# Optimization experiments

Hardware: AMD Instinct MI355X
Metric: run time of the kernel (lower is better)

Reference implementation:

```python
import jax, jax.numpy as jnp
import numpy as np

B, C, W, H = 16, 256, 32, 32
HEAD, NREG = 4, 1
D = C // HEAD
N = W * H


def setup_inputs() -> dict:
    key = jax.random.key(0)
    ks = jax.random.split(key, 11)
    return {
        "x": jax.random.normal(ks[0], (B, C, W, H), jnp.float32),
        "Wq": jax.random.normal(ks[1], (C, C), jnp.float32) * 0.05,
        "bq": jax.random.normal(ks[2], (C,), jnp.float32) * 0.05,
        "Wk": jax.random.normal(ks[3], (C, C), jnp.float32) * 0.05,
        "bk": jax.random.normal(ks[4], (C,), jnp.float32) * 0.05,
        "Wv": jax.random.normal(ks[5], (C, C), jnp.float32) * 0.05,
        "bv": jax.random.normal(ks[6], (C,), jnp.float32) * 0.05,
        "rel_h": jax.random.normal(ks[7], (1, HEAD, D, 1, H), jnp.float32),
        "rel_w": jax.random.normal(ks[8], (1, HEAD, D, W, 1), jnp.float32),
        "reg_qk": jax.random.normal(ks[9], (NREG, N, N), jnp.float32),
        "reg_v": jax.random.normal(ks[10], (NREG, D, N), jnp.float32),
    }


def reference(x, Wq, bq, Wk, bk, Wv, bv, rel_h, rel_w, reg_qk, reg_v):
    b, c, w, h = x.shape
    head = rel_h.shape[1]
    d = c // head
    n = w * h
    xf = x.reshape(b, c, n)  # flatten spatial; 1x1 conv == channel matmul
    q = (jnp.einsum('oc,bcn->bon', Wq, xf) + bq[:, None]).reshape(b, head, d, n)
    k = (jnp.einsum('oc,bcn->bon', Wk, xf) + bk[:, None]).reshape(b, head, d, n)
    v = (jnp.einsum('oc,bcn->bon', Wv, xf) + bv[:, None]).reshape(b, head, d, n)
    # content-content: q^T k -> [b, head, n, n]
    cc = jnp.einsum('bhdn,bhdm->bhnm', q, k)
    # relative position: (rel_h + rel_w) broadcast-summed to [1,head,d,w,h] -> [head,d,n]
    pos = (rel_h + rel_w).reshape(head, d, n)
    # pos^T @ q -> [b, head, n, n]
    cp = jnp.einsum('hdn,bhdm->bhnm', pos, q)
    energy = cc + cp  # [b, head, n, n]
    # pack register tokens along the head axis
    energy = jnp.concatenate(
        [energy, jnp.broadcast_to(reg_qk[None], (b,) + reg_qk.shape)], axis=1)
    vcat = jnp.concatenate(
        [v, jnp.broadcast_to(reg_v[None], (b,) + reg_v.shape)], axis=1)
    attn = jax.nn.softmax(energy, axis=-1)  # [b, head+nreg, n, n]
    # out = v @ attn^T : [b, g, d, n]
    out = jnp.einsum('bgdn,bgmn->bgdm', vcat, attn)
    # unpack: keep only the real heads
    out = out[:, :head].reshape(b, c, w, h)
    return out
```

## Files before the change

### kernel.cpp

```cpp
#include <hip/hip_runtime.h>

#define BB 16
#define CH 256
#define NH 4
#define DH 64
#define NN 1024

typedef _Float16 f16x8 __attribute__((ext_vector_type(8)));
typedef float f32x4 __attribute__((ext_vector_type(4)));
typedef float f32x16 __attribute__((ext_vector_type(16)));
typedef unsigned int uint32x4 __attribute__((ext_vector_type(4)));

__device__ __forceinline__ unsigned short f2h(float x) {
    _Float16 h = (_Float16)x;
    return __builtin_bit_cast(unsigned short, h);
}

__device__ __forceinline__ unsigned cvtpk(float a, float b) {
    auto r = __builtin_amdgcn_cvt_pkrtz(a, b);
    return __builtin_bit_cast(unsigned, r);
}

__global__ __launch_bounds__(256) void prep_kernel(
    const float* __restrict__ Wq, const float* __restrict__ Wk, const float* __restrict__ Wv,
    unsigned short* __restrict__ Wh)
{
    int idx = blockIdx.x * 256 + threadIdx.x;
    if (idx >= 3 * CH * CH) return;
    int p = idx >> 16, oc = idx & 65535;
    const float* W = (p == 0) ? Wq : ((p == 1) ? Wk : Wv);
    Wh[idx] = f2h(W[oc]);
}

__global__ __launch_bounds__(256) void xt_kernel(
    const float* __restrict__ x, unsigned short* __restrict__ xT)
{
    const int b = blockIdx.z, c0 = blockIdx.y * 32, n0 = blockIdx.x * 32;
    __shared__ float T[32][33];
    const int t = threadIdx.x;
    {
        int c = t >> 3, n4 = (t & 7) * 4;
        float4 v4 = *(const float4*)&x[((size_t)b * CH + c0 + c) * NN + n0 + n4];
        T[c][n4 + 0] = v4.x; T[c][n4 + 1] = v4.y;
        T[c][n4 + 2] = v4.z; T[c][n4 + 3] = v4.w;
    }
    __syncthreads();
    {
        int n = t >> 3, c4 = (t & 7) * 4;
        ushort4 o;
        o.x = f2h(T[c4 + 0][n]); o.y = f2h(T[c4 + 1][n]);
        o.z = f2h(T[c4 + 2][n]); o.w = f2h(T[c4 + 3][n]);
        *(ushort4*)&xT[((size_t)b * NN + n0 + n) * CH + c0 + c4] = o;
    }
}

__global__ __launch_bounds__(256) void pos_kernel(
    const float* __restrict__ rel_h, const float* __restrict__ rel_w,
    unsigned short* __restrict__ pT)
{
    int idx = blockIdx.x * 256 + threadIdx.x;
    if (idx >= NH * NN * DH) return;
    int d = idx & 63, n = (idx >> 6) & (NN - 1), h = idx >> 16;
    float val = rel_w[(h * DH + d) * 32 + (n >> 5)] + rel_h[(h * DH + d) * 32 + (n & 31)];
    pT[idx] = f2h(val);
}

__global__ __launch_bounds__(256) void proj_kernel(
    const unsigned short* __restrict__ xT,
    const unsigned short* __restrict__ Wh,
    const float* __restrict__ bq, const float* __restrict__ bk, const float* __restrict__ bv,
    unsigned short* __restrict__ kF, unsigned short* __restrict__ vF)
{
    const int bz = blockIdx.z;
    const int b = bz / 3, p = bz % 3;
    const int jt = blockIdx.x;
    const int ot = blockIdx.y;
    const int n0 = jt * 64;
    const int o0 = ot * 64;
    const float* bias = (p == 0) ? bq : ((p == 1) ? bk : bv);

    __shared__ __align__(16) unsigned short Xs[64][72];
    __shared__ __align__(16) unsigned short Whs[64][72];
    __shared__ __align__(16) unsigned short Img[8192];

    const int tid = threadIdx.x;
    const int wid = tid >> 6, lane = tid & 63;
    const int g = lane >> 4, lr = lane & 15;
    const int l31 = lane & 31, hi = lane >> 5;

    const unsigned short* xb  = xT + (size_t)b * NN * CH;
    const unsigned short* Whp = Wh + (size_t)p * CH * CH;

    const f32x4 z4 = {0.f, 0.f, 0.f, 0.f};
    f32x4 acc[4] = {z4, z4, z4, z4};

    for (int cs = 0; cs < 4; ++cs) {
        const int c0 = cs * 64;
        __syncthreads();
        #pragma unroll
        for (int rep = 0; rep < 2; ++rep) {
            int f = rep * 256 + tid;
            int r = f >> 3, s = f & 7;
            *(uint4*)&Xs[r][s * 8]  = *(const uint4*)&xb[(size_t)(n0 + r) * CH + c0 + s * 8];
            *(uint4*)&Whs[r][s * 8] = *(const uint4*)&Whp[(size_t)(o0 + r) * CH + c0 + s * 8];
        }
        __syncthreads();
        #pragma unroll
        for (int ks = 0; ks < 2; ++ks) {
            f16x8 ah = *(const f16x8*)&Whs[wid * 16 + lr][ks * 32 + g * 8];
            #pragma unroll
            for (int fc = 0; fc < 4; ++fc) {
                f16x8 bx = *(const f16x8*)&Xs[fc * 16 + lr][ks * 32 + g * 8];
                acc[fc] = __builtin_amdgcn_mfma_f32_16x16x32_f16(ah, bx, acc[fc], 0, 0, 0);
            }
        }
    }

    float bb[4];
    #pragma unroll
    for (int rr = 0; rr < 4; ++rr) bb[rr] = bias[o0 + wid * 16 + g * 4 + rr];

    const int bh = b * NH + ot;

    if (p < 2) {
        const float scale = (p == 0) ? 1.44269504088896f : 1.0f;
        const int qoff = (p == 0) ? 8 : 0;
        #pragma unroll
        for (int fc = 0; fc < 4; ++fc)
            #pragma unroll
            for (int rr = 0; rr < 4; ++rr) {
                int jl = fc * 16 + lr;
                int dd = wid * 16 + g * 4 + rr;
                Img[jl * 128 + ((((dd >> 3) + qoff) ^ (jl & 15)) << 3) + (dd & 7)] =
                    f2h((acc[fc][rr] + bb[rr]) * scale);
            }
        __syncthreads();
        const int ks = ((p == 0) ? 4 : 0) + wid;
        #pragma unroll
        for (int grp = 0; grp < 2; ++grp) {
            int row = grp * 32 + l31;
            int slot = ks * 2 + hi;
            uint4 v = *(const uint4*)&Img[row * 128 + ((slot ^ (row & 15)) << 3)];
            size_t dst = ((((size_t)bh * 16 + jt) * 8 + ks) * 2 + grp) * 512 + (size_t)lane * 8;
            *(uint4*)&kF[dst] = v;
        }
    } else {
        #pragma unroll
        for (int fc = 0; fc < 4; ++fc)
            #pragma unroll
            for (int rr = 0; rr < 4; ++rr) {
                int d  = wid * 16 + g * 4 + rr;
                int jl = fc * 16 + lr;
                int vc = jl >> 3, c4 = (jl >> 2) & 1, c = jl & 3;
                int vM = ((vc >> 1) << 2) + (vc & 1) + ((d >> 5) << 4);
                Img[(d & 31) * 128 + ((((vM >> 1) + c4) ^ (d & 15)) << 3) + ((vM & 1) << 2) + c] =
                    f2h(acc[fc][rr] + bb[rr]);
            }
        __syncthreads();
        const int u = wid;
        #pragma unroll
        for (int which = 0; which < 2; ++which) {
            int slot = which * 8 + u * 2 + hi;
            int row = l31;
            uint4 v = *(const uint4*)&Img[row * 128 + ((slot ^ (row & 15)) << 3)];
            size_t dst = ((((size_t)bh * 16 + jt) * 4 + u) * 2 + which) * 512 + (size_t)lane * 8;
            *(uint4*)&vF[dst] = v;
        }
    }
}

__global__ __launch_bounds__(256, 2) void attn_kernel(
    const unsigned short* __restrict__ pT,
    const unsigned short* __restrict__ kF, const unsigned short* __restrict__ vF,
    float* __restrict__ out)
{
    const int wg = blockIdx.x;
    const int bh = (wg & 7) * 8 + ((wg >> 3) & 7);
    const int it = wg >> 6;
    const int b = bh >> 2, h = bh & 3;
    const int i0 = it * 128;

    __shared__ __align__(16) float Epi[64 * 132];
    __shared__ __align__(16) float Lbuf[128];
    __shared__ float ScBuf[4][32];

    const int tid = threadIdx.x;
    const int wid = tid >> 6, lane = tid & 63;
    const int l31 = lane & 31, hi = lane >> 5;

    const unsigned short* pTb = pT + (size_t)h * NN * DH;

    const unsigned short* kFb = kF + (size_t)bh * 16 * 8192 + (size_t)lane * 8;
    const unsigned short* vFb = vF + (size_t)bh * 16 * 4096 + (size_t)lane * 8;

    f16x8 bQ[8];
    {
        const int i = i0 + wid * 32 + l31;
        const unsigned short* qck = kFb + (size_t)(it * 2 + (wid >> 1)) * 8192;
        #pragma unroll
        for (int ksp = 0; ksp < 4; ++ksp) {
            bQ[ksp] = *(const f16x8*)(qck + (((4 + ksp) * 2 + (wid & 1)) * 512));
            bQ[4 + ksp] = *(const f16x8*)&pTb[(size_t)i * DH + ksp * 16 + hi * 8];
        }
    }

    f32x16 O0 = {}, O1 = {};
    float m_run = -1e30f, l_run = 0.f;

    for (int t = 0; t < 16; ++t) {
        const unsigned short* kt = kFb + (size_t)t * 8192;
        const unsigned short* vt = vFb + (size_t)t * 4096;

        f16x8 a0[8], a1[8];
        #pragma unroll
        for (int ks = 0; ks < 8; ++ks) {
            a0[ks] = *(const f16x8*)(kt + ks * 1024);
            a1[ks] = *(const f16x8*)(kt + ks * 1024 + 512);
        }
        f16x8 vf0[4], vf1[4];
        #pragma unroll
        for (int u = 0; u < 4; ++u) {
            vf0[u] = *(const f16x8*)(vt + u * 1024);
            vf1[u] = *(const f16x8*)(vt + u * 1024 + 512);
        }

        f32x16 s0 = {}, s1 = {};
        __builtin_amdgcn_s_setprio(1);
        #pragma unroll
        for (int ks = 0; ks < 8; ++ks) {
            s0 = __builtin_amdgcn_mfma_f32_32x32x16_f16(a0[ks], bQ[ks], s0, 0, 0, 0);
            s1 = __builtin_amdgcn_mfma_f32_32x32x16_f16(a1[ks], bQ[ks], s1, 0, 0, 0);
        }
        __builtin_amdgcn_s_setprio(0);

        float fm = s0[0];
        #pragma unroll
        for (int r = 1; r < 16; ++r) fm = fmaxf(fm, s0[r]);
        #pragma unroll
        for (int r = 0; r < 16; ++r) fm = fmaxf(fm, s1[r]);

        if (!__all(fm <= m_run + 8.f)) {
            float fmf = fmaxf(fm, __shfl_xor(fm, 32));
            float mn = fmaxf(m_run, fmf);
            float sc = exp2f(m_run - mn);
            m_run = mn;
            l_run *= sc;
            if (lane < 32) ScBuf[wid][lane] = sc;
            #pragma unroll
            for (int r = 0; r < 16; ++r) {
                int irow = (r & 3) + 8 * (r >> 2) + 4 * hi;
                float scv = ScBuf[wid][irow];
                O0[r] *= scv; O1[r] *= scv;
            }
        }

        unsigned c0[8], c1[8];
        float ps = 0.f;
        #pragma unroll
        for (int m = 0; m < 8; ++m) {
            float pa = exp2f(s0[2 * m]     - m_run);
            float pb = exp2f(s0[2 * m + 1] - m_run);
            float pc = exp2f(s1[2 * m]     - m_run);
            float pd = exp2f(s1[2 * m + 1] - m_run);
            ps += (pa + pb) + (pc + pd);
            c0[m] = cvtpk(pa, pb);
            c1[m] = cvtpk(pc, pd);
        }
        l_run += ps;

        f16x8 pA[2][2];
        #pragma unroll
        for (int js = 0; js < 2; ++js) {
            unsigned* c = js ? c1 : c0;
            #pragma unroll
            for (int ksi = 0; ksi < 2; ++ksi) {
                uint32x4 w = { c[ksi * 4 + 0], c[ksi * 4 + 1], c[ksi * 4 + 2], c[ksi * 4 + 3] };
                pA[js][ksi] = __builtin_bit_cast(f16x8, w);
            }
        }

        __builtin_amdgcn_s_setprio(1);
        #pragma unroll
        for (int js = 0; js < 2; ++js) {
            #pragma unroll
            for (int ksi = 0; ksi < 2; ++ksi) {
                int u = js * 2 + ksi;
                O0 = __builtin_amdgcn_mfma_f32_32x32x16_f16(pA[js][ksi], vf0[u], O0, 0, 0, 0);
                O1 = __builtin_amdgcn_mfma_f32_32x32x16_f16(pA[js][ksi], vf1[u], O1, 0, 0, 0);
            }
        }
        __builtin_amdgcn_s_setprio(0);
    }

    float l_full = l_run + __shfl_xor(l_run, 32);
    float invl = 1.0f / l_full;
    if (lane < 32) Lbuf[wid * 32 + lane] = invl;
    #pragma unroll
    for (int r = 0; r < 16; ++r) {
        int irow = (r & 3) + 8 * (r >> 2) + 4 * hi;
        int ilocal = wid * 32 + irow;
        Epi[(l31) * 132 + ilocal]      = O0[r];
        Epi[(32 + l31) * 132 + ilocal] = O1[r];
    }
    __syncthreads();
    float* ob = out + ((size_t)b * CH + h * DH) * NN + i0;
    #pragma unroll
    for (int rep = 0; rep < 8; ++rep) {
        int f = rep * 256 + tid;
        int d = f >> 5, q = f & 31;
        float4 v4 = *(const float4*)&Epi[d * 132 + q * 4];
        float4 iv = *(const float4*)&Lbuf[q * 4];
        v4.x *= iv.x; v4.y *= iv.y; v4.z *= iv.z; v4.w *= iv.w;
        *(float4*)&ob[(size_t)d * NN + q * 4] = v4;
    }
}

extern "C" void kernel_launch(void* const* d_in, const int* in_sizes, int n_in,
                              void* d_out, int out_size, void* d_ws, size_t ws_size,
                              hipStream_t stream) {
    const float* x     = (const float*)d_in[0];
    const float* Wq    = (const float*)d_in[1];
    const float* bq    = (const float*)d_in[2];
    const float* Wk    = (const float*)d_in[3];
    const float* bk    = (const float*)d_in[4];
    const float* Wv    = (const float*)d_in[5];
    const float* bv    = (const float*)d_in[6];
    const float* rel_h = (const float*)d_in[7];
    const float* rel_w = (const float*)d_in[8];
    float* out = (float*)d_out;

    unsigned short* kF = (unsigned short*)d_ws;
    unsigned short* vF = kF + (size_t)8388608;
    unsigned short* pT = vF + (size_t)4194304;
    unsigned short* xT = pT + (size_t)262144;
    unsigned short* Wh = xT + (size_t)4194304;

    prep_kernel<<<dim3((3 * CH * CH + 255) / 256), 256, 0, stream>>>(Wq, Wk, Wv, Wh);
    xt_kernel<<<dim3(NN / 32, CH / 32, BB), 256, 0, stream>>>(x, xT);
    pos_kernel<<<dim3((NH * NN * DH + 255) / 256), 256, 0, stream>>>(rel_h, rel_w, pT);
    proj_kernel<<<dim3(NN / 64, CH / 64, BB * 3), 256, 0, stream>>>(
        xT, Wh, bq, bk, bv, kF, vF);
    attn_kernel<<<dim3(512), 256, 0, stream>>>(pT, kF, vF, out);
}
```

Measured before the change: 78.85 us.

## Fuse weight conversion and position embedding into projection and attention kernels

Removes the separate weight fp16 conversion and position-table kernels. The projection kernel now converts fp32 weights on the fly and computes Q, K and V for one x tile in a single block. That block loads its x tile once into a larger shared buffer and reuses it across all three projections. The attention kernel builds the position fragment directly from rel_h/rel_w. This cuts two launches and the x reloads, but each projection block does three times the work, launches a third as many blocks, and issues scattered scalar loads for the position terms.

```diff
diff --git a/kernel.cpp b/kernel.cpp
--- a/kernel.cpp
+++ b/kernel.cpp
@@ -19,17 +19,6 @@
 __device__ __forceinline__ unsigned cvtpk(float a, float b) {
     auto r = __builtin_amdgcn_cvt_pkrtz(a, b);
     return __builtin_bit_cast(unsigned, r);
-}
-
-__global__ __launch_bounds__(256) void prep_kernel(
-    const float* __restrict__ Wq, const float* __restrict__ Wk, const float* __restrict__ Wv,
-    unsigned short* __restrict__ Wh)
-{
-    int idx = blockIdx.x * 256 + threadIdx.x;
-    if (idx >= 3 * CH * CH) return;
-    int p = idx >> 16, oc = idx & 65535;
-    const float* W = (p == 0) ? Wq : ((p == 1) ? Wk : Wv);
-    Wh[idx] = f2h(W[oc]);
 }
 
 __global__ __launch_bounds__(256) void xt_kernel(
@@ -54,124 +43,130 @@
     }
 }
 
-__global__ __launch_bounds__(256) void pos_kernel(
-    const float* __restrict__ rel_h, const float* __restrict__ rel_w,
-    unsigned short* __restrict__ pT)
-{
-    int idx = blockIdx.x * 256 + threadIdx.x;
-    if (idx >= NH * NN * DH) return;
-    int d = idx & 63, n = (idx >> 6) & (NN - 1), h = idx >> 16;
-    float val = rel_w[(h * DH + d) * 32 + (n >> 5)] + rel_h[(h * DH + d) * 32 + (n & 31)];
-    pT[idx] = f2h(val);
-}
-
 __global__ __launch_bounds__(256) void proj_kernel(
     const unsigned short* __restrict__ xT,
-    const unsigned short* __restrict__ Wh,
+    const float* __restrict__ Wq, const float* __restrict__ Wk, const float* __restrict__ Wv,
     const float* __restrict__ bq, const float* __restrict__ bk, const float* __restrict__ bv,
     unsigned short* __restrict__ kF, unsigned short* __restrict__ vF)
 {
-    const int bz = blockIdx.z;
-    const int b = bz / 3, p = bz % 3;
     const int jt = blockIdx.x;
     const int ot = blockIdx.y;
-    const int n0 = jt * 64;
-    const int o0 = ot * 64;
-    const float* bias = (p == 0) ? bq : ((p == 1) ? bk : bv);
-
-    __shared__ __align__(16) unsigned short Xs[64][72];
-    __shared__ __align__(16) unsigned short Whs[64][72];
-    __shared__ __align__(16) unsigned short Img[8192];
+    const int b  = blockIdx.z;
+    const int n0 = jt * 64, o0 = ot * 64;
+
+    __shared__ __align__(16) unsigned short Xs[64][264];
+    __shared__ __align__(16) unsigned short WhImg[8192];
+    unsigned short (*Whs)[72] = (unsigned short (*)[72])WhImg;
+    unsigned short* Img = WhImg;
 
     const int tid = threadIdx.x;
     const int wid = tid >> 6, lane = tid & 63;
     const int g = lane >> 4, lr = lane & 15;
     const int l31 = lane & 31, hi = lane >> 5;
 
-    const unsigned short* xb  = xT + (size_t)b * NN * CH;
-    const unsigned short* Whp = Wh + (size_t)p * CH * CH;
-
+    const unsigned short* xb = xT + (size_t)b * NN * CH;
+
+    #pragma unroll
+    for (int rep = 0; rep < 8; ++rep) {
+        int f = rep * 256 + tid;
+        int n = f >> 5, s = f & 31;
+        *(uint4*)&Xs[n][s * 8] = *(const uint4*)&xb[(size_t)(n0 + n) * CH + s * 8];
+    }
+
+    const int bh = b * NH + ot;
     const f32x4 z4 = {0.f, 0.f, 0.f, 0.f};
-    f32x4 acc[4] = {z4, z4, z4, z4};
-
-    for (int cs = 0; cs < 4; ++cs) {
-        const int c0 = cs * 64;
+
+    for (int p = 0; p < 3; ++p) {
+        const float* Wp   = (p == 0) ? Wq : ((p == 1) ? Wk : Wv);
+        const float* bias = (p == 0) ? bq : ((p == 1) ? bk : bv);
+
+        f32x4 acc[4] = {z4, z4, z4, z4};
+
+        for (int cs = 0; cs < 4; ++cs) {
+            const int c0 = cs * 64;
+            __syncthreads();
+            #pragma unroll
+            for (int rep = 0; rep < 2; ++rep) {
+                int f = rep * 256 + tid;
+                int r = f >> 3, s = f & 7;
+                const float* src = &Wp[(size_t)(o0 + r) * CH + c0 + s * 8];
+                float4 w0 = *(const float4*)src;
+                float4 w1 = *(const float4*)(src + 4);
+                ushort4 ha, hb;
+                ha.x = f2h(w0.x); ha.y = f2h(w0.y); ha.z = f2h(w0.z); ha.w = f2h(w0.w);
+                hb.x = f2h(w1.x); hb.y = f2h(w1.y); hb.z = f2h(w1.z); hb.w = f2h(w1.w);
+                *(ushort4*)&Whs[r][s * 8]     = ha;
+                *(ushort4*)&Whs[r][s * 8 + 4] = hb;
+            }
+            __syncthreads();
+            #pragma unroll
+            for (int ks = 0; ks < 2; ++ks) {
+                f16x8 ah = *(const f16x8*)&Whs[wid * 16 + lr][ks * 32 + g * 8];
+                #pragma unroll
+                for (int fc = 0; fc < 4; ++fc) {
+                    f16x8 bx = *(const f16x8*)&Xs[fc * 16 + lr][c0 + ks * 32 + g * 8];
+                    acc[fc] = __builtin_amdgcn_mfma_f32_16x16x32_f16(ah, bx, acc[fc], 0, 0, 0);
+                }
+            }
+        }
+
+        float bb[4];
+        #pragma unroll
+        for (int rr = 0; rr < 4; ++rr) bb[rr] = bias[o0 + wid * 16 + g * 4 + rr];
+
         __syncthreads();
-        #pragma unroll
-        for (int rep = 0; rep < 2; ++rep) {
-            int f = rep * 256 + tid;
-            int r = f >> 3, s = f & 7;
-            *(uint4*)&Xs[r][s * 8]  = *(const uint4*)&xb[(size_t)(n0 + r) * CH + c0 + s * 8];
-            *(uint4*)&Whs[r][s * 8] = *(const uint4*)&Whp[(size_t)(o0 + r) * CH + c0 + s * 8];
-        }
-        __syncthreads();
-        #pragma unroll
-        for (int ks = 0; ks < 2; ++ks) {
-            f16x8 ah = *(const f16x8*)&Whs[wid * 16 + lr][ks * 32 + g * 8];
-            #pragma unroll
-            for (int fc = 0; fc < 4; ++fc) {
-                f16x8 bx = *(const f16x8*)&Xs[fc * 16 + lr][ks * 32 + g * 8];
-                acc[fc] = __builtin_amdgcn_mfma_f32_16x16x32_f16(ah, bx, acc[fc], 0, 0, 0);
-            }
-        }
-    }
-
-    float bb[4];
-    #pragma unroll
-    for (int rr = 0; rr < 4; ++rr) bb[rr] = bias[o0 + wid * 16 + g * 4 + rr];
-
-    const int bh = b * NH + ot;
-
-    if (p < 2) {
-        const float scale = (p == 0) ? 1.44269504088896f : 1.0f;
-        const int qoff = (p == 0) ? 8 : 0;
-        #pragma unroll
-        for (int fc = 0; fc < 4; ++fc)
-            #pragma unroll
-            for (int rr = 0; rr < 4; ++rr) {
-                int jl = fc * 16 + lr;
-                int dd = wid * 16 + g * 4 + rr;
-                Img[jl * 128 + ((((dd >> 3) + qoff) ^ (jl & 15)) << 3) + (dd & 7)] =
-                    f2h((acc[fc][rr] + bb[rr]) * scale);
-            }
-        __syncthreads();
-        const int ks = ((p == 0) ? 4 : 0) + wid;
-        #pragma unroll
-        for (int grp = 0; grp < 2; ++grp) {
-            int row = grp * 32 + l31;
-            int slot = ks * 2 + hi;
-            uint4 v = *(const uint4*)&Img[row * 128 + ((slot ^ (row & 15)) << 3)];
-            size_t dst = ((((size_t)bh * 16 + jt) * 8 + ks) * 2 + grp) * 512 + (size_t)lane * 8;
-            *(uint4*)&kF[dst] = v;
-        }
-    } else {
-        #pragma unroll
-        for (int fc = 0; fc < 4; ++fc)
-            #pragma unroll
-            for (int rr = 0; rr < 4; ++rr) {
-                int d  = wid * 16 + g * 4 + rr;
-                int jl = fc * 16 + lr;
-                int vc = jl >> 3, c4 = (jl >> 2) & 1, c = jl & 3;
-                int vM = ((vc >> 1) << 2) + (vc & 1) + ((d >> 5) << 4);
-                Img[(d & 31) * 128 + ((((vM >> 1) + c4) ^ (d & 15)) << 3) + ((vM & 1) << 2) + c] =
-                    f2h(acc[fc][rr] + bb[rr]);
-            }
-        __syncthreads();
-        const int u = wid;
-        #pragma unroll
-        for (int which = 0; which < 2; ++which) {
-            int slot = which * 8 + u * 2 + hi;
-            int row = l31;
-            uint4 v = *(const uint4*)&Img[row * 128 + ((slot ^ (row & 15)) << 3)];
-            size_t dst = ((((size_t)bh * 16 + jt) * 4 + u) * 2 + which) * 512 + (size_t)lane * 8;
-            *(uint4*)&vF[dst] = v;
+
+        if (p < 2) {
+            const float scale = (p == 0) ? 1.44269504088896f : 1.0f;
+            const int qoff = (p == 0) ? 8 : 0;
+            #pragma unroll
+            for (int fc = 0; fc < 4; ++fc)
+                #pragma unroll
+                for (int rr = 0; rr < 4; ++rr) {
+                    int jl = fc * 16 + lr;
+                    int dd = wid * 16 + g * 4 + rr;
+                    Img[jl * 128 + ((((dd >> 3) + qoff) ^ (jl & 15)) << 3) + (dd & 7)] =
+                        f2h((acc[fc][rr] + bb[rr]) * scale);
+                }
+            __syncthreads();
+            const int ks = ((p == 0) ? 4 : 0) + wid;
+            #pragma unroll
+            for (int grp = 0; grp < 2; ++grp) {
+                int row = grp * 32 + l31;
+                int slot = ks * 2 + hi;
+                uint4 v = *(const uint4*)&Img[row * 128 + ((slot ^ (row & 15)) << 3)];
+                size_t dst = ((((size_t)bh * 16 + jt) * 8 + ks) * 2 + grp) * 512 + (size_t)lane * 8;
+                *(uint4*)&kF[dst] = v;
+            }
+        } else {
+            #pragma unroll
+            for (int fc = 0; fc < 4; ++fc)
+                #pragma unroll
+                for (int rr = 0; rr < 4; ++rr) {
+                    int d  = wid * 16 + g * 4 + rr;
+                    int jl = fc * 16 + lr;
+                    int vc = jl >> 3, c4 = (jl >> 2) & 1, c = jl & 3;
+                    int vM = ((vc >> 1) << 2) + (vc & 1) + ((d >> 5) << 4);
+                    Img[(d & 31) * 128 + ((((vM >> 1) + c4) ^ (d & 15)) << 3) + ((vM & 1) << 2) + c] =
+                        f2h(acc[fc][rr] + bb[rr]);
+                }
+            __syncthreads();
+            const int u = wid;
+            #pragma unroll
+            for (int which = 0; which < 2; ++which) {
+                int slot = which * 8 + u * 2 + hi;
+                int row = l31;
+                uint4 v = *(const uint4*)&Img[row * 128 + ((slot ^ (row & 15)) << 3)];
+                size_t dst = ((((size_t)bh * 16 + jt) * 4 + u) * 2 + which) * 512 + (size_t)lane * 8;
+                *(uint4*)&vF[dst] = v;
+            }
         }
     }
 }
 
 __global__ __launch_bounds__(256, 2) void attn_kernel(
-    const unsigned short* __restrict__ pT,
     const unsigned short* __restrict__ kF, const unsigned short* __restrict__ vF,
+    const float* __restrict__ rel_h, const float* __restrict__ rel_w,
     float* __restrict__ out)
 {
     const int wg = blockIdx.x;
@@ -188,19 +183,25 @@
     const int wid = tid >> 6, lane = tid & 63;
     const int l31 = lane & 31, hi = lane >> 5;
 
-    const unsigned short* pTb = pT + (size_t)h * NN * DH;
-
     const unsigned short* kFb = kF + (size_t)bh * 16 * 8192 + (size_t)lane * 8;
     const unsigned short* vFb = vF + (size_t)bh * 16 * 4096 + (size_t)lane * 8;
 
     f16x8 bQ[8];
     {
         const int i = i0 + wid * 32 + l31;
+        const int iw = i >> 5, ih = i & 31;
         const unsigned short* qck = kFb + (size_t)(it * 2 + (wid >> 1)) * 8192;
         #pragma unroll
         for (int ksp = 0; ksp < 4; ++ksp) {
             bQ[ksp] = *(const f16x8*)(qck + (((4 + ksp) * 2 + (wid & 1)) * 512));
-            bQ[4 + ksp] = *(const f16x8*)&pTb[(size_t)i * DH + ksp * 16 + hi * 8];
+            int d0 = ksp * 16 + hi * 8;
+            f16x8 pp;
+            #pragma unroll
+            for (int e = 0; e < 8; ++e) {
+                int d = d0 + e;
+                pp[e] = (_Float16)(rel_w[(h * 64 + d) * 32 + iw] + rel_h[(h * 64 + d) * 32 + ih]);
+            }
+            bQ[4 + ksp] = pp;
         }
     }
 
@@ -331,14 +332,10 @@
 
     unsigned short* kF = (unsigned short*)d_ws;
     unsigned short* vF = kF + (size_t)8388608;
-    unsigned short* pT = vF + (size_t)4194304;
-    unsigned short* xT = pT + (size_t)262144;
-    unsigned short* Wh = xT + (size_t)4194304;
-
-    prep_kernel<<<dim3((3 * CH * CH + 255) / 256), 256, 0, stream>>>(Wq, Wk, Wv, Wh);
+    unsigned short* xT = vF + (size_t)4194304;
+
     xt_kernel<<<dim3(NN / 32, CH / 32, BB), 256, 0, stream>>>(x, xT);
-    pos_kernel<<<dim3((NH * NN * DH + 255) / 256), 256, 0, stream>>>(rel_h, rel_w, pT);
-    proj_kernel<<<dim3(NN / 64, CH / 64, BB * 3), 256, 0, stream>>>(
-        xT, Wh, bq, bk, bv, kF, vF);
-    attn_kernel<<<dim3(512), 256, 0, stream>>>(pT, kF, vF, out);
-}
+    proj_kernel<<<dim3(16, 4, 16), 256, 0, stream>>>(
+        xT, Wq, Wk, Wv, bq, bk, bv, kF, vF);
+    attn_kernel<<<dim3(512), 256, 0, stream>>>(kF, vF, rel_h, rel_w, out);
+}
```

Result: slower. 82.73 us (+4.9%).

## Split attention key range across two wave groups and fuse positional embedding

Applied to the files above, without the earlier changes.

The attention kernel now launches 512 threads per block. Two groups of four waves each process half of the key tiles, and their partial softmax states (max, sum, output) are merged through shared memory, like a split-K flash-decoding combine. The separate pos_kernel is removed and the rel_h + rel_w sum is computed directly into registers at attention start. The aim is more waves in flight per block to hide latency and one fewer launch, at the cost of extra LDS merge traffic, extra barriers, and possibly higher register pressure under the new launch bounds.

```diff
diff --git a/kernel.cpp b/kernel.cpp
--- a/kernel.cpp
+++ b/kernel.cpp
@@ -52,17 +52,6 @@
         o.z = f2h(T[c4 + 2][n]); o.w = f2h(T[c4 + 3][n]);
         *(ushort4*)&xT[((size_t)b * NN + n0 + n) * CH + c0 + c4] = o;
     }
-}
-
-__global__ __launch_bounds__(256) void pos_kernel(
-    const float* __restrict__ rel_h, const float* __restrict__ rel_w,
-    unsigned short* __restrict__ pT)
-{
-    int idx = blockIdx.x * 256 + threadIdx.x;
-    if (idx >= NH * NN * DH) return;
-    int d = idx & 63, n = (idx >> 6) & (NN - 1), h = idx >> 16;
-    float val = rel_w[(h * DH + d) * 32 + (n >> 5)] + rel_h[(h * DH + d) * 32 + (n & 31)];
-    pT[idx] = f2h(val);
 }
 
 __global__ __launch_bounds__(256) void proj_kernel(
@@ -121,6 +110,7 @@
     for (int rr = 0; rr < 4; ++rr) bb[rr] = bias[o0 + wid * 16 + g * 4 + rr];
 
     const int bh = b * NH + ot;
+    __syncthreads();
 
     if (p < 2) {
         const float scale = (p == 0) ? 1.44269504088896f : 1.0f;
@@ -169,9 +159,9 @@
     }
 }
 
-__global__ __launch_bounds__(256, 2) void attn_kernel(
-    const unsigned short* __restrict__ pT,
+__global__ __launch_bounds__(512, 4) void attn_kernel(
     const unsigned short* __restrict__ kF, const unsigned short* __restrict__ vF,
+    const float* __restrict__ rel_h, const float* __restrict__ rel_w,
     float* __restrict__ out)
 {
     const int wg = blockIdx.x;
@@ -182,32 +172,44 @@
 
     __shared__ __align__(16) float Epi[64 * 132];
     __shared__ __align__(16) float Lbuf[128];
-    __shared__ float ScBuf[4][32];
+    __shared__ float ScBuf[8][32];
+    __shared__ float ScA[4][32], ScB[4][32];
+    __shared__ float MBuf[4][32];
+    __shared__ float LpBuf[4][64];
 
     const int tid = threadIdx.x;
     const int wid = tid >> 6, lane = tid & 63;
+    const int wpair = wid & 3, jhalf = wid >> 2;
     const int l31 = lane & 31, hi = lane >> 5;
-
-    const unsigned short* pTb = pT + (size_t)h * NN * DH;
 
     const unsigned short* kFb = kF + (size_t)bh * 16 * 8192 + (size_t)lane * 8;
     const unsigned short* vFb = vF + (size_t)bh * 16 * 4096 + (size_t)lane * 8;
 
     f16x8 bQ[8];
     {
-        const int i = i0 + wid * 32 + l31;
-        const unsigned short* qck = kFb + (size_t)(it * 2 + (wid >> 1)) * 8192;
+        const int i = i0 + wpair * 32 + l31;
+        const int iw = i >> 5, ih = i & 31;
+        const unsigned short* qck = kFb + (size_t)(it * 2 + (wpair >> 1)) * 8192;
         #pragma unroll
         for (int ksp = 0; ksp < 4; ++ksp) {
-            bQ[ksp] = *(const f16x8*)(qck + (((4 + ksp) * 2 + (wid & 1)) * 512));
-            bQ[4 + ksp] = *(const f16x8*)&pTb[(size_t)i * DH + ksp * 16 + hi * 8];
+            bQ[ksp] = *(const f16x8*)(qck + (((4 + ksp) * 2 + (wpair & 1)) * 512));
+            int d0 = ksp * 16 + hi * 8;
+            f16x8 pp;
+            #pragma unroll
+            for (int e = 0; e < 8; ++e) {
+                int d = d0 + e;
+                pp[e] = (_Float16)(rel_w[(h * 64 + d) * 32 + iw] + rel_h[(h * 64 + d) * 32 + ih]);
+            }
+            bQ[4 + ksp] = pp;
         }
     }
 
     f32x16 O0 = {}, O1 = {};
     float m_run = -1e30f, l_run = 0.f;
 
-    for (int t = 0; t < 16; ++t) {
+    const int t0 = jhalf * 8;
+    for (int tt = 0; tt < 8; ++tt) {
+        const int t = t0 + tt;
         const unsigned short* kt = kFb + (size_t)t * 8192;
         const unsigned short* vt = vFb + (size_t)t * 4096;
 
@@ -292,21 +294,50 @@
         __builtin_amdgcn_s_setprio(0);
     }
 
-    float l_full = l_run + __shfl_xor(l_run, 32);
-    float invl = 1.0f / l_full;
-    if (lane < 32) Lbuf[wid * 32 + lane] = invl;
-    #pragma unroll
-    for (int r = 0; r < 16; ++r) {
-        int irow = (r & 3) + 8 * (r >> 2) + 4 * hi;
-        int ilocal = wid * 32 + irow;
-        Epi[(l31) * 132 + ilocal]      = O0[r];
-        Epi[(32 + l31) * 132 + ilocal] = O1[r];
+    float* OBuf = Epi;
+    if (jhalf == 1) {
+        if (lane < 32) MBuf[wpair][lane] = m_run;
+        LpBuf[wpair][lane] = l_run;
+        #pragma unroll
+        for (int r = 0; r < 16; ++r) {
+            OBuf[(wpair * 32 + r) * 64 + lane]      = O0[r];
+            OBuf[(wpair * 32 + 16 + r) * 64 + lane] = O1[r];
+        }
+    }
+    __syncthreads();
+    if (jhalf == 0) {
+        float m_b = MBuf[wpair][l31];
+        float mm = fmaxf(m_run, m_b);
+        float sa = exp2f(m_run - mm), sb = exp2f(m_b - mm);
+        if (lane < 32) { ScA[wpair][lane] = sa; ScB[wpair][lane] = sb; }
+        l_run = l_run * sa + LpBuf[wpair][lane] * sb;
+        #pragma unroll
+        for (int r = 0; r < 16; ++r) {
+            int irow = (r & 3) + 8 * (r >> 2) + 4 * hi;
+            float sA = ScA[wpair][irow], sB = ScB[wpair][irow];
+            O0[r] = O0[r] * sA + OBuf[(wpair * 32 + r) * 64 + lane] * sB;
+            O1[r] = O1[r] * sA + OBuf[(wpair * 32 + 16 + r) * 64 + lane] * sB;
+        }
+    }
+    __syncthreads();
+
+    if (jhalf == 0) {
+        float l_full = l_run + __shfl_xor(l_run, 32);
+        float invl = 1.0f / l_full;
+        if (lane < 32) Lbuf[wpair * 32 + lane] = invl;
+        #pragma unroll
+        for (int r = 0; r < 16; ++r) {
+            int irow = (r & 3) + 8 * (r >> 2) + 4 * hi;
+            int ilocal = wpair * 32 + irow;
+            Epi[(l31) * 132 + ilocal]      = O0[r];
+            Epi[(32 + l31) * 132 + ilocal] = O1[r];
+        }
     }
     __syncthreads();
     float* ob = out + ((size_t)b * CH + h * DH) * NN + i0;
     #pragma unroll
-    for (int rep = 0; rep < 8; ++rep) {
-        int f = rep * 256 + tid;
+    for (int rep = 0; rep < 4; ++rep) {
+        int f = rep * 512 + tid;
         int d = f >> 5, q = f & 31;
         float4 v4 = *(const float4*)&Epi[d * 132 + q * 4];
         float4 iv = *(const float4*)&Lbuf[q * 4];
@@ -331,14 +362,12 @@
 
     unsigned short* kF = (unsigned short*)d_ws;
     unsigned short* vF = kF + (size_t)8388608;
-    unsigned short* pT = vF + (size_t)4194304;
-    unsigned short* xT = pT + (size_t)262144;
+    unsigned short* xT = vF + (size_t)4194304;
     unsigned short* Wh = xT + (size_t)4194304;
 
     prep_kernel<<<dim3((3 * CH * CH + 255) / 256), 256, 0, stream>>>(Wq, Wk, Wv, Wh);
     xt_kernel<<<dim3(NN / 32, CH / 32, BB), 256, 0, stream>>>(x, xT);
-    pos_kernel<<<dim3((NH * NN * DH + 255) / 256), 256, 0, stream>>>(rel_h, rel_w, pT);
-    proj_kernel<<<dim3(NN / 64, CH / 64, BB * 3), 256, 0, stream>>>(
+    proj_kernel<<<dim3(16, 4, 48), 256, 0, stream>>>(
         xT, Wh, bq, bk, bv, kF, vF);
-    attn_kernel<<<dim3(512), 256, 0, stream>>>(pT, kF, vF, out);
-}
+    attn_kernel<<<dim3(512), 512, 0, stream>>>(kF, vF, rel_h, rel_w, out);
+}
```

After: 228.8 us. 2.9x slower.
